# Kernel optimization log

Measured on AMD Instinct MI355X. Metric: run time of the kernel, lower is better.

Reference implementation:

```python
import jax, jax.numpy as jnp
import numpy as np

N_NODES = 4096
N_EDGES = 131072
F_DIM = 16
H_DIM = 32

def _mlp_params(key, in_dim, hidden):
    ks = jax.random.split(key, 6)
    s1 = 1.0 / np.sqrt(in_dim); s2 = 1.0 / np.sqrt(hidden)
    return dict(
        W1=jax.random.uniform(ks[0], (in_dim, hidden), jnp.float32, -s1, s1),
        b1=jax.random.uniform(ks[1], (hidden,), jnp.float32, -s1, s1),
        W2=jax.random.uniform(ks[2], (hidden, hidden), jnp.float32, -s2, s2),
        b2=jax.random.uniform(ks[3], (hidden,), jnp.float32, -s2, s2),
        W3=jax.random.uniform(ks[4], (hidden, 1), jnp.float32, -s2, s2),
        b3=jax.random.uniform(ks[5], (1,), jnp.float32, -s2, s2),
    )

def _mlp(x, W1, b1, W2, b2, W3, b3):
    h = jax.nn.relu(x @ W1 + b1)
    h = jax.nn.relu(h @ W2 + b2)
    return (h @ W3 + b3)[..., 0]  # (E,)

def setup_inputs() -> dict:
    key = jax.random.key(0)
    k_ei, k_ef, k_s, k_p = jax.random.split(key, 4)
    edge_index = jax.random.randint(k_ei, (N_EDGES, 2), 0, N_NODES, dtype=jnp.int32)
    edge_feat = jax.random.normal(k_ef, (N_EDGES, F_DIM), dtype=jnp.float32)
    sh = _mlp_params(k_s, F_DIM, H_DIM)
    sp = _mlp_params(k_p, F_DIM, H_DIM)
    return dict(
        species_idx=0,
        edge_index=edge_index,
        edge_feat=edge_feat,
        num_nodes=N_NODES,
        sW1=sh['W1'], sb1=sh['b1'], sW2=sh['W2'], sb2=sh['b2'], sW3=sh['W3'], sb3=sh['b3'],
        pW1=sp['W1'], pb1=sp['b1'], pW2=sp['W2'], pb2=sp['b2'], pW3=sp['W3'], pb3=sp['b3'],
    )

def reference(species_idx, edge_index, edge_feat, num_nodes,
              sW1, sb1, sW2, sb2, sW3, sb3,
              pW1, pb1, pW2, pb2, pW3, pb3):
    # Edge logits: shared head + species head (species_idx selects the head;
    # here the selected head's params are passed directly).
    shared = _mlp(edge_feat, sW1, sb1, sW2, sb2, sW3, sb3)   # (E,)
    species = _mlp(edge_feat, pW1, pb1, pW2, pb2, pW3, pb3)  # (E,)
    resistance = jax.nn.softplus(shared + species) + 1e-4
    conductance = 1.0 / resistance
    i = edge_index[:, 0]
    j = edge_index[:, 1]
    # Scatter-assembled graph Laplacian (N x N)
    L = jnp.zeros((num_nodes, num_nodes), dtype=edge_feat.dtype)
    L = L.at[i, i].add(conductance)
    L = L.at[j, j].add(conductance)
    L = L.at[i, j].add(-conductance)
    L = L.at[j, i].add(-conductance)
    L_pinv = jnp.linalg.pinv(L)
    diag = jnp.diagonal(L_pinv)
    R = diag[:, None] + diag[None, :] - 2.0 * L_pinv
    return R, shared, species
```

## Files before the change

### kernel.cpp

```cpp
#include <hip/hip_runtime.h>
#include <hip/hip_bf16.h>


#define NN 4096
#define LDA 4096
#define NEDGE 131072
#define INVN (1.0f/4096.0f)

__device__ __forceinline__ float mlp_eval(const float* __restrict__ w,
                                          const float* __restrict__ x) {
  float h1[32], h2[32];
#pragma unroll
  for (int o = 0; o < 32; o += 4) {
    float4 s = *(const float4*)&w[512 + o];
#pragma unroll
    for (int i = 0; i < 16; ++i) {
      float4 wv = *(const float4*)&w[i * 32 + o];
      s.x = fmaf(x[i], wv.x, s.x); s.y = fmaf(x[i], wv.y, s.y);
      s.z = fmaf(x[i], wv.z, s.z); s.w = fmaf(x[i], wv.w, s.w);
    }
    h1[o] = fmaxf(s.x, 0.f); h1[o+1] = fmaxf(s.y, 0.f);
    h1[o+2] = fmaxf(s.z, 0.f); h1[o+3] = fmaxf(s.w, 0.f);
  }
#pragma unroll
  for (int o = 0; o < 32; o += 4) {
    float4 s = *(const float4*)&w[1568 + o];
#pragma unroll
    for (int i = 0; i < 32; ++i) {
      float4 wv = *(const float4*)&w[544 + i * 32 + o];
      s.x = fmaf(h1[i], wv.x, s.x); s.y = fmaf(h1[i], wv.y, s.y);
      s.z = fmaf(h1[i], wv.z, s.z); s.w = fmaf(h1[i], wv.w, s.w);
    }
    h2[o] = fmaxf(s.x, 0.f); h2[o+1] = fmaxf(s.y, 0.f);
    h2[o+2] = fmaxf(s.z, 0.f); h2[o+3] = fmaxf(s.w, 0.f);
  }
  float out = w[1632];
#pragma unroll
  for (int i = 0; i < 32; ++i) out = fmaf(h2[i], w[1600 + i], out);
  return out;
}

__global__ __launch_bounds__(256) void mlp_kernel(
    const float* __restrict__ ef,
    const float* __restrict__ sW1, const float* __restrict__ sb1,
    const float* __restrict__ sW2, const float* __restrict__ sb2,
    const float* __restrict__ sW3, const float* __restrict__ sb3,
    const float* __restrict__ pW1, const float* __restrict__ pb1,
    const float* __restrict__ pW2, const float* __restrict__ pb2,
    const float* __restrict__ pW3, const float* __restrict__ pb3,
    float* __restrict__ outS, float* __restrict__ outP,
    float* __restrict__ cond) {
  __shared__ float w[3328];
  int t = threadIdx.x;
  for (int i = t; i < 512; i += 256) { w[i] = sW1[i]; w[1664 + i] = pW1[i]; }
  for (int i = t; i < 1024; i += 256) { w[544 + i] = sW2[i]; w[1664 + 544 + i] = pW2[i]; }
  if (t < 32) {
    w[512 + t] = sb1[t]; w[1568 + t] = sb2[t]; w[1600 + t] = sW3[t];
    w[1664 + 512 + t] = pb1[t]; w[1664 + 1568 + t] = pb2[t]; w[1664 + 1600 + t] = pW3[t];
  }
  if (t == 0) { w[1632] = sb3[0]; w[1664 + 1632] = pb3[0]; }
  __syncthreads();
  int e = blockIdx.x * 256 + t;
  float x[16];
#pragma unroll
  for (int i = 0; i < 16; i += 4) {
    float4 v = *(const float4*)&ef[(size_t)e * 16 + i];
    x[i] = v.x; x[i+1] = v.y; x[i+2] = v.z; x[i+3] = v.w;
  }
  float s = mlp_eval(w, x);
  float p = mlp_eval(w + 1664, x);
  outS[e] = s; outP[e] = p;
  float z = s + p;
  float sp = fmaxf(z, 0.f) + log1pf(expf(-fabsf(z)));
  cond[e] = 1.0f / (sp + 1e-4f);
}

__global__ __launch_bounds__(256) void init_A(float* __restrict__ A) {
  size_t q = (size_t)blockIdx.x * 256 + threadIdx.x;
  *(float4*)&A[q * 4] = make_float4(INVN, INVN, INVN, INVN);
}

__global__ __launch_bounds__(256) void zero_ws(float* __restrict__ P) {
  size_t q = (size_t)blockIdx.x * 256 + threadIdx.x;
  *(float4*)&P[q * 4] = make_float4(0.f, 0.f, 0.f, 0.f);
}

__global__ __launch_bounds__(256) void scatter_kernel(const int* __restrict__ ei,
                                                      const float* __restrict__ cond,
                                                      float* __restrict__ A) {
  int e = blockIdx.x * 256 + threadIdx.x;
  int i = ei[2 * e], j = ei[2 * e + 1];
  float c = cond[e];
  atomicAdd(&A[(size_t)i * (LDA + 1)], c);
  atomicAdd(&A[(size_t)j * (LDA + 1)], c);
  atomicAdd(&A[(size_t)i * LDA + j], -c);
  atomicAdd(&A[(size_t)j * LDA + i], -c);
}

__device__ __forceinline__ float rlane(float v, int l) {
  return __int_as_float(__builtin_amdgcn_readlane(__float_as_int(v), l));
}

__device__ __noinline__ void potf2_dev(float* __restrict__ A, int kt, int lane,
                                       float (* __restrict__ GT)[68]) {
  float* blk = A + (size_t)kt * 64 * (LDA + 1);
  float a[64], x[64];
#pragma unroll
  for (int c = 0; c < 64; c += 4) {
    float4 v = *(const float4*)&blk[(size_t)lane * LDA + c];
    a[c] = v.x; a[c+1] = v.y; a[c+2] = v.z; a[c+3] = v.w;
    x[c]   = (c   == lane) ? 1.f : 0.f;
    x[c+1] = (c+1 == lane) ? 1.f : 0.f;
    x[c+2] = (c+2 == lane) ? 1.f : 0.f;
    x[c+3] = (c+3 == lane) ? 1.f : 0.f;
  }
#pragma unroll
  for (int j = 0; j < 64; ++j) {
    float dj = rlane(a[j], j);
    float inv = 1.0f / sqrtf(dj);
    float lij = a[j] * inv;
    a[j] = lij;
    float coefT = -lij;
    float sX = (lane == j) ? inv : 1.0f;
    float coefX = (lane > j) ? -lij : 0.0f;
#pragma unroll
    for (int c = j + 1; c < 64; ++c)
      a[c] = fmaf(coefT, rlane(lij, c), a[c]);
#pragma unroll
    for (int c = 0; c <= j; ++c) {
      float xjc = rlane(x[c], j) * inv;
      x[c] = fmaf(coefX, xjc, x[c] * sX);
    }
  }
#pragma unroll
  for (int c = 0; c < 64; c += 4)
    *(float4*)&blk[(size_t)lane * LDA + c] = make_float4(a[c], a[c+1], a[c+2], a[c+3]);
#pragma unroll
  for (int c = 0; c < 64; ++c) GT[c][lane] = x[c];
}

__device__ __forceinline__ void syrk_tile(float* __restrict__ A, int t0, int ti_, int tj_,
                                          const float (* __restrict__ LtA)[68],
                                          const float (* __restrict__ LtB)[68], int gtid) {
  int tx = gtid & 15, ty = gtid >> 4;
  float acc[4][4] = {};
  for (int k = 0; k < 64; ++k) {
    float4 a4 = *(const float4*)&LtA[k][ty * 4];
    float4 b4 = *(const float4*)&LtB[k][tx * 4];
    float aa[4] = {a4.x, a4.y, a4.z, a4.w};
    float bb[4] = {b4.x, b4.y, b4.z, b4.w};
#pragma unroll
    for (int i = 0; i < 4; ++i)
#pragma unroll
      for (int jj = 0; jj < 4; ++jj) acc[i][jj] = fmaf(aa[i], bb[jj], acc[i][jj]);
  }
  float* C = A + ((size_t)(t0 + ti_) * 64) * LDA + (size_t)(t0 + tj_) * 64;
#pragma unroll
  for (int i = 0; i < 4; ++i) {
    float* p = &C[(size_t)(ty * 4 + i) * LDA + tx * 4];
    float4 c = *(float4*)p;
    c.x -= acc[i][0]; c.y -= acc[i][1]; c.z -= acc[i][2]; c.w -= acc[i][3];
    *(float4*)p = c;
  }
}

__global__ __launch_bounds__(512) void potrf_diag256(float* __restrict__ A,
                                                     float* __restrict__ GinvAll,
                                                     int p) {
  __shared__ float GT[64][68];
  __shared__ float At[2][64][68];
  __shared__ float Lt[3][64][68];
  int tid = threadIdx.x;
  int wid = tid >> 6, lane = tid & 63;
  int grp = tid >> 8, gtid = tid & 255;
  int t0 = p * 4;
  for (int kk = 0; kk < 4; ++kk) {
    if (wid == 0) {
      potf2_dev(A, t0 + kk, lane, GT);
    } else if (grp == 1) {
      const int TI_[5] = {2, 3, 2, 3, 3};
      const int TJ_[5] = {1, 1, 2, 2, 3};
#pragma unroll 5
      for (int t = 0; t < 5; ++t) {
        bool on = (kk == 1) || (kk == 2 && t >= 3);
        if (on)
          syrk_tile(A, t0, TI_[t], TJ_[t], Lt[TI_[t] - kk], Lt[TJ_[t] - kk], gtid);
      }
    }
    __syncthreads();
    {
      int base = (t0 + kk) * 4096;
#pragma unroll 8
      for (int u = 0; u < 8; ++u) {
        int q = tid * 8 + u;
        GinvAll[base + q] = GT[q & 63][q >> 6];
      }
    }
    for (int rnd = 0; rnd < 2; ++rnd) {
      int it = kk + 1 + rnd * 2 + grp;
      bool act = (it <= 3);
      if (act) {
        for (int q = gtid; q < 1024; q += 256) {
          int r = q >> 4, k4 = (q & 15) << 2;
          float4 v = *(const float4*)&A[((size_t)(t0 + it) * 64 + r) * LDA +
                                        (size_t)(t0 + kk) * 64 + k4];
          At[grp][k4 + 0][r] = v.x; At[grp][k4 + 1][r] = v.y;
          At[grp][k4 + 2][r] = v.z; At[grp][k4 + 3][r] = v.w;
        }
      }
      __syncthreads();
      if (act) {
        int tx = gtid & 15, ty = gtid >> 4;
        float acc[4][4] = {};
        for (int k = 0; k < 64; ++k) {
          float4 a4 = *(const float4*)&At[grp][k][ty * 4];
          float4 b4 = *(const float4*)&GT[k][tx * 4];
          float aa[4] = {a4.x, a4.y, a4.z, a4.w};
          float bb[4] = {b4.x, b4.y, b4.z, b4.w};
#pragma unroll
          for (int i = 0; i < 4; ++i)
#pragma unroll
            for (int jj = 0; jj < 4; ++jj) acc[i][jj] = fmaf(aa[i], bb[jj], acc[i][jj]);
        }
        int s = it - kk - 1;
#pragma unroll
        for (int jj = 0; jj < 4; ++jj)
          *(float4*)&Lt[s][tx * 4 + jj][ty * 4] =
              make_float4(acc[0][jj], acc[1][jj], acc[2][jj], acc[3][jj]);
        float* C = A + ((size_t)(t0 + it) * 64) * LDA + (size_t)(t0 + kk) * 64;
#pragma unroll
        for (int i = 0; i < 4; ++i)
          *(float4*)&C[(size_t)(ty * 4 + i) * LDA + tx * 4] =
              make_float4(acc[i][0], acc[i][1], acc[i][2], acc[i][3]);
      }
      __syncthreads();
    }
    if (kk < 3 && grp == 0)
      syrk_tile(A, t0, kk + 1, kk + 1, Lt[0], Lt[0], gtid);
    __syncthreads();
  }
}

__global__ __launch_bounds__(256) void trsm_panel256(float* __restrict__ A,
                                                     const float* __restrict__ GinvAll,
                                                     int p) {
  __shared__ float Sr[64][260];
  __shared__ float Bt[64][68];
  int tid = threadIdx.x;
  int c0 = p * 256;
  int r0 = c0 + 256 + blockIdx.x * 64;
  for (int q = tid; q < 4096; q += 256) {
    int r = q >> 6, c4 = (q & 63) << 2;
    *(float4*)&Sr[r][c4] = *(const float4*)&A[(size_t)(r0 + r) * LDA + c0 + c4];
  }
  __syncthreads();
  int tx = tid & 15, ty = tid >> 4;
  for (int j = 0; j < 4; ++j) {
    float acc2[4][4] = {};
    for (int p2 = 0; p2 < j; ++p2) {
      for (int q = tid; q < 1024; q += 256) {
        int c = q >> 4, k4 = (q & 15) << 2;
        float4 v = *(const float4*)&A[(size_t)(c0 + j * 64 + c) * LDA +
                                      c0 + p2 * 64 + k4];
        Bt[k4 + 0][c] = v.x; Bt[k4 + 1][c] = v.y;
        Bt[k4 + 2][c] = v.z; Bt[k4 + 3][c] = v.w;
      }
      __syncthreads();
      for (int k = 0; k < 64; ++k) {
        float a0 = Sr[ty * 4 + 0][p2 * 64 + k];
        float a1 = Sr[ty * 4 + 1][p2 * 64 + k];
        float a2 = Sr[ty * 4 + 2][p2 * 64 + k];
        float a3 = Sr[ty * 4 + 3][p2 * 64 + k];
        float4 b = *(const float4*)&Bt[k][tx * 4];
        acc2[0][0] = fmaf(a0, b.x, acc2[0][0]); acc2[0][1] = fmaf(a0, b.y, acc2[0][1]);
        acc2[0][2] = fmaf(a0, b.z, acc2[0][2]); acc2[0][3] = fmaf(a0, b.w, acc2[0][3]);
        acc2[1][0] = fmaf(a1, b.x, acc2[1][0]); acc2[1][1] = fmaf(a1, b.y, acc2[1][1]);
        acc2[1][2] = fmaf(a1, b.z, acc2[1][2]); acc2[1][3] = fmaf(a1, b.w, acc2[1][3]);
        acc2[2][0] = fmaf(a2, b.x, acc2[2][0]); acc2[2][1] = fmaf(a2, b.y, acc2[2][1]);
        acc2[2][2] = fmaf(a2, b.z, acc2[2][2]); acc2[2][3] = fmaf(a2, b.w, acc2[2][3]);
        acc2[3][0] = fmaf(a3, b.x, acc2[3][0]); acc2[3][1] = fmaf(a3, b.y, acc2[3][1]);
        acc2[3][2] = fmaf(a3, b.z, acc2[3][2]); acc2[3][3] = fmaf(a3, b.w, acc2[3][3]);
      }
      __syncthreads();
    }
    if (j > 0) {
#pragma unroll
      for (int i = 0; i < 4; ++i) {
        Sr[ty * 4 + i][j * 64 + tx * 4 + 0] -= acc2[i][0];
        Sr[ty * 4 + i][j * 64 + tx * 4 + 1] -= acc2[i][1];
        Sr[ty * 4 + i][j * 64 + tx * 4 + 2] -= acc2[i][2];
        Sr[ty * 4 + i][j * 64 + tx * 4 + 3] -= acc2[i][3];
      }
    }
    __syncthreads();
    {
      const float* G = GinvAll + (size_t)(p * 4 + j) * 4096;
      for (int q = tid; q < 1024; q += 256) {
        int c = q >> 4, k4 = (q & 15) << 2;
        float4 v = *(const float4*)&G[c * 64 + k4];
        Bt[k4 + 0][c] = v.x; Bt[k4 + 1][c] = v.y;
        Bt[k4 + 2][c] = v.z; Bt[k4 + 3][c] = v.w;
      }
    }
    __syncthreads();
    float acc3[4][4] = {};
    for (int k = 0; k < 64; ++k) {
      float a0 = Sr[ty * 4 + 0][j * 64 + k];
      float a1 = Sr[ty * 4 + 1][j * 64 + k];
      float a2 = Sr[ty * 4 + 2][j * 64 + k];
      float a3 = Sr[ty * 4 + 3][j * 64 + k];
      float4 b = *(const float4*)&Bt[k][tx * 4];
      acc3[0][0] = fmaf(a0, b.x, acc3[0][0]); acc3[0][1] = fmaf(a0, b.y, acc3[0][1]);
      acc3[0][2] = fmaf(a0, b.z, acc3[0][2]); acc3[0][3] = fmaf(a0, b.w, acc3[0][3]);
      acc3[1][0] = fmaf(a1, b.x, acc3[1][0]); acc3[1][1] = fmaf(a1, b.y, acc3[1][1]);
      acc3[1][2] = fmaf(a1, b.z, acc3[1][2]); acc3[1][3] = fmaf(a1, b.w, acc3[1][3]);
      acc3[2][0] = fmaf(a2, b.x, acc3[2][0]); acc3[2][1] = fmaf(a2, b.y, acc3[2][1]);
      acc3[2][2] = fmaf(a2, b.z, acc3[2][2]); acc3[2][3] = fmaf(a2, b.w, acc3[2][3]);
      acc3[3][0] = fmaf(a3, b.x, acc3[3][0]); acc3[3][1] = fmaf(a3, b.y, acc3[3][1]);
      acc3[3][2] = fmaf(a3, b.z, acc3[3][2]); acc3[3][3] = fmaf(a3, b.w, acc3[3][3]);
    }
    __syncthreads();
#pragma unroll
    for (int i = 0; i < 4; ++i) {
      Sr[ty * 4 + i][j * 64 + tx * 4 + 0] = acc3[i][0];
      Sr[ty * 4 + i][j * 64 + tx * 4 + 1] = acc3[i][1];
      Sr[ty * 4 + i][j * 64 + tx * 4 + 2] = acc3[i][2];
      Sr[ty * 4 + i][j * 64 + tx * 4 + 3] = acc3[i][3];
    }
    __syncthreads();
  }
  for (int q = tid; q < 4096; q += 256) {
    int r = q >> 6, c4 = (q & 63) << 2;
    *(float4*)&A[(size_t)(r0 + r) * LDA + c0 + c4] = *(float4*)&Sr[r][c4];
  }
}

template <bool TA, bool TB, bool ACCUM, bool LOWER, bool KST, bool CCOMP>
__global__ __launch_bounds__(256) void gemm64(
    const float* __restrict__ Ab, long long aZ, int lda,
    const float* __restrict__ Bb, long long bZ, int ldb,
    float* __restrict__ Cb, long long cZ, int ldc, int K, float alpha) {
  int ti = blockIdx.x, tj = blockIdx.y;
  if (LOWER && tj > ti) return;
  const float* A = Ab + (long long)blockIdx.z * aZ;
  const float* B = Bb + (long long)blockIdx.z * bZ;
  __shared__ float As[16][68], Bs[16][68];
  int tid = threadIdx.x;
  int tx = tid & 15, ty = tid >> 4;
  float acc[4][4] = {};
  int m0 = ti * 64, n0 = tj * 64;
  int k0 = KST ? ti * 64 : 0;
  for (int k = k0; k < K; k += 16) {
    if (!TA) {
      int r = tid >> 2, c4 = (tid & 3) * 4;
      float4 v = *(const float4*)&A[(size_t)(m0 + r) * lda + k + c4];
      As[c4 + 0][r] = v.x; As[c4 + 1][r] = v.y; As[c4 + 2][r] = v.z; As[c4 + 3][r] = v.w;
    } else {
      int r = tid >> 4, c4 = (tid & 15) * 4;
      *(float4*)&As[r][c4] = *(const float4*)&A[(size_t)(k + r) * lda + m0 + c4];
    }
    if (TB) {
      int r = tid >> 2, c4 = (tid & 3) * 4;
      float4 v = *(const float4*)&B[(size_t)(n0 + r) * ldb + k + c4];
      Bs[c4 + 0][r] = v.x; Bs[c4 + 1][r] = v.y; Bs[c4 + 2][r] = v.z; Bs[c4 + 3][r] = v.w;
    } else {
      int r = tid >> 4, c4 = (tid & 15) * 4;
      *(float4*)&Bs[r][c4] = *(const float4*)&B[(size_t)(k + r) * ldb + n0 + c4];
    }
    __syncthreads();
#pragma unroll
    for (int kk = 0; kk < 16; ++kk) {
      float4 av = *(const float4*)&As[kk][ty * 4];
      float4 bv = *(const float4*)&Bs[kk][tx * 4];
      float a[4] = {av.x, av.y, av.z, av.w};
      float b[4] = {bv.x, bv.y, bv.z, bv.w};
#pragma unroll
      for (int i = 0; i < 4; ++i)
#pragma unroll
        for (int jj = 0; jj < 4; ++jj) acc[i][jj] = fmaf(a[i], b[jj], acc[i][jj]);
    }
    __syncthreads();
  }
  float* C = Cb + (long long)blockIdx.z * cZ;
#pragma unroll
  for (int i = 0; i < 4; ++i) {
    size_t off = (size_t)(m0 + ty * 4 + i) * ldc + n0 + tx * 4;
    float4 c;
    if (ACCUM) {
      c = *(float4*)&C[off];
      c.x += alpha * acc[i][0]; c.y += alpha * acc[i][1];
      c.z += alpha * acc[i][2]; c.w += alpha * acc[i][3];
    } else {
      c.x = alpha * acc[i][0]; c.y = alpha * acc[i][1];
      c.z = alpha * acc[i][2]; c.w = alpha * acc[i][3];
    }
    *(float4*)&C[off] = c;
  }
}

template <bool TA, bool TB, bool ACCUM, bool TRI, bool KST, bool CCOMP,
          bool ATOMIC, bool KSPLIT>
__global__ __launch_bounds__(256) void gemm128(
    const float* __restrict__ Ab, long long aZ, int lda,
    const float* __restrict__ Bb, long long bZ, int ldb,
    float* __restrict__ Cb, long long cZ, int ldc, int K, float alpha) {
  int ti, tj;
  if (TRI) {
    int bid = blockIdx.x;
    ti = (int)((sqrtf(8.0f * bid + 1.0f) - 1.0f) * 0.5f);
    while ((ti + 1) * (ti + 2) / 2 <= bid) ++ti;
    while (ti * (ti + 1) / 2 > bid) --ti;
    tj = bid - ti * (ti + 1) / 2;
  } else {
    ti = blockIdx.x; tj = blockIdx.y;
  }
  int k0 = KST ? ti * 128 : 0;
  int kEnd = K;
  if (KSPLIT) {
    if (blockIdx.z == 0) { kEnd = 2048; if (k0 >= kEnd) return; }
    else { k0 = (k0 > 2048) ? k0 : 2048; }
  }
  const float* A = KSPLIT ? Ab : Ab + (long long)blockIdx.z * aZ;
  const float* B = KSPLIT ? Bb : Bb + (long long)blockIdx.z * bZ;
  __shared__ float As[16][132], Bs[16][132];
  int tid = threadIdx.x;
  int tx = tid & 15, ty = tid >> 4;
  float acc[8][8] = {};
  int m0 = ti * 128, n0 = tj * 128;
  for (int k = k0; k < kEnd; k += 16) {
    if (!TA) {
      int r = tid >> 1, c8 = (tid & 1) * 8;
      const float* src = &A[(size_t)(m0 + r) * lda + k + c8];
      float4 v0 = *(const float4*)src;
      float4 v1 = *(const float4*)(src + 4);
      As[c8 + 0][r] = v0.x; As[c8 + 1][r] = v0.y; As[c8 + 2][r] = v0.z; As[c8 + 3][r] = v0.w;
      As[c8 + 4][r] = v1.x; As[c8 + 5][r] = v1.y; As[c8 + 6][r] = v1.z; As[c8 + 7][r] = v1.w;
    } else {
      int r = tid >> 4, c8 = (tid & 15) * 8;
      const float* src = &A[(size_t)(k + r) * lda + m0 + c8];
      *(float4*)&As[r][c8]     = *(const float4*)src;
      *(float4*)&As[r][c8 + 4] = *(const float4*)(src + 4);
    }
    if (TB) {
      int r = tid >> 1, c8 = (tid & 1) * 8;
      const float* src = &B[(size_t)(n0 + r) * ldb + k + c8];
      float4 v0 = *(const float4*)src;
      float4 v1 = *(const float4*)(src + 4);
      Bs[c8 + 0][r] = v0.x; Bs[c8 + 1][r] = v0.y; Bs[c8 + 2][r] = v0.z; Bs[c8 + 3][r] = v0.w;
      Bs[c8 + 4][r] = v1.x; Bs[c8 + 5][r] = v1.y; Bs[c8 + 6][r] = v1.z; Bs[c8 + 7][r] = v1.w;
    } else {
      int r = tid >> 4, c8 = (tid & 15) * 8;
      const float* src = &B[(size_t)(k + r) * ldb + n0 + c8];
      *(float4*)&Bs[r][c8]     = *(const float4*)src;
      *(float4*)&Bs[r][c8 + 4] = *(const float4*)(src + 4);
    }
    __syncthreads();
#pragma unroll
    for (int kk = 0; kk < 16; ++kk) {
      float a8[8], b8[8];
      *(float4*)&a8[0] = *(const float4*)&As[kk][ty * 4];
      *(float4*)&a8[4] = *(const float4*)&As[kk][64 + ty * 4];
      *(float4*)&b8[0] = *(const float4*)&Bs[kk][tx * 4];
      *(float4*)&b8[4] = *(const float4*)&Bs[kk][64 + tx * 4];
#pragma unroll
      for (int i = 0; i < 8; ++i)
#pragma unroll
        for (int jj = 0; jj < 8; ++jj) acc[i][jj] = fmaf(a8[i], b8[jj], acc[i][jj]);
    }
    __syncthreads();
  }
  if (CCOMP) {
#pragma unroll
    for (int hr = 0; hr < 2; ++hr) {
      int TI = 2 * ti + hr;
#pragma unroll
      for (int hc = 0; hc < 2; ++hc) {
        int TJ = 2 * tj + hc;
        if (TJ > TI) continue;
        float* C = Cb + ((size_t)TI * (TI + 1) / 2 + TJ) * 4096;
#pragma unroll
        for (int i = 0; i < 4; ++i) {
          if (ATOMIC) {
            float* pbase = &C[(ty * 4 + i) * 64 + tx * 4];
            atomicAdd(pbase + 0, alpha * acc[hr * 4 + i][hc * 4 + 0]);
            atomicAdd(pbase + 1, alpha * acc[hr * 4 + i][hc * 4 + 1]);
            atomicAdd(pbase + 2, alpha * acc[hr * 4 + i][hc * 4 + 2]);
            atomicAdd(pbase + 3, alpha * acc[hr * 4 + i][hc * 4 + 3]);
          } else {
            float4 c;
            c.x = alpha * acc[hr * 4 + i][hc * 4 + 0];
            c.y = alpha * acc[hr * 4 + i][hc * 4 + 1];
            c.z = alpha * acc[hr * 4 + i][hc * 4 + 2];
            c.w = alpha * acc[hr * 4 + i][hc * 4 + 3];
            *(float4*)&C[(ty * 4 + i) * 64 + tx * 4] = c;
          }
        }
      }
    }
  } else {
    float* C = Cb + (long long)blockIdx.z * cZ;
#pragma unroll
    for (int i = 0; i < 8; ++i) {
      int row = (i < 4) ? (m0 + ty * 4 + i) : (m0 + 64 + ty * 4 + i - 4);
      float* dst0 = &C[(size_t)row * ldc + n0 + tx * 4];
      float* dst1 = dst0 + 64;
      float4 c0, c1;
      c0.x = alpha * acc[i][0]; c0.y = alpha * acc[i][1];
      c0.z = alpha * acc[i][2]; c0.w = alpha * acc[i][3];
      c1.x = alpha * acc[i][4]; c1.y = alpha * acc[i][5];
      c1.z = alpha * acc[i][6]; c1.w = alpha * acc[i][7];
      if (ACCUM) {
        float4 o0 = *(float4*)dst0, o1 = *(float4*)dst1;
        c0.x += o0.x; c0.y += o0.y; c0.z += o0.z; c0.w += o0.w;
        c1.x += o1.x; c1.y += o1.y; c1.z += o1.z; c1.w += o1.w;
      }
      *(float4*)dst0 = c0;
      *(float4*)dst1 = c1;
    }
  }
}

__global__ __launch_bounds__(256) void finish_W_prep(float* __restrict__ A,
                                                     const float* __restrict__ GinvAll) {
  size_t q = (size_t)blockIdx.x * 256 + threadIdx.x;
  int r = (int)(q >> 10), c4 = (int)(q & 1023) << 2;
  int rb = r >> 6, cb = c4 >> 6;
  if (cb == rb) {
    const float* g = GinvAll + (size_t)rb * 4096 + (size_t)(r & 63) * 64 + (c4 & 63);
    *(float4*)&A[q * 4] = *(const float4*)g;
  } else if (cb > rb) {
    *(float4*)&A[q * 4] = make_float4(0.f, 0.f, 0.f, 0.f);
  }
}

__global__ __launch_bounds__(256) void copy_diag(const float* __restrict__ Mc,
                                                 float* __restrict__ d) {
  int i = blockIdx.x * 256 + threadIdx.x;
  int tb = i >> 6;
  size_t q = (size_t)tb * (tb + 1) / 2 + tb;
  d[i] = Mc[q * 4096 + (size_t)(i & 63) * 65];
}

__global__ __launch_bounds__(256) void final_R(const float* __restrict__ Mc,
                                               const float* __restrict__ d,
                                               float* __restrict__ out) {
  size_t idx = (size_t)blockIdx.x * 256 + threadIdx.x;
  int r = (int)(idx >> 12), c = (int)(idx & 4095);
  int a = r > c ? r : c, b = r > c ? c : r;
  int ta = a >> 6, tb = b >> 6;
  size_t q = (size_t)ta * (ta + 1) / 2 + tb;
  float m = Mc[q * 4096 + (size_t)(a & 63) * 64 + (b & 63)];
  out[idx] = d[r] + d[c] - 2.0f * m;
}

extern "C" void kernel_launch(void* const* d_in, const int* in_sizes, int n_in,
                              void* d_out, int out_size, void* d_ws, size_t ws_size,
                              hipStream_t stream) {
  const int* eidx = (const int*)d_in[1];
  const float* ef = (const float*)d_in[2];
  const float* sW1 = (const float*)d_in[4],  *sb1 = (const float*)d_in[5];
  const float* sW2 = (const float*)d_in[6],  *sb2 = (const float*)d_in[7];
  const float* sW3 = (const float*)d_in[8],  *sb3 = (const float*)d_in[9];
  const float* pW1 = (const float*)d_in[10], *pb1 = (const float*)d_in[11];
  const float* pW2 = (const float*)d_in[12], *pb2 = (const float*)d_in[13];
  const float* pW3 = (const float*)d_in[14], *pb3 = (const float*)d_in[15];

  float* dout = (float*)d_out;
  float* dA = dout;
  float* outS = dout + (size_t)NN * NN;
  float* outP = outS + NEDGE;

  float* ws = (float*)d_ws;
  float* Mc = ws;
  float* U = ws + 8519680ull;
  float* cond = U;
  float* Ginv = U;
  float* Tbuf = U;
  float* diagb = U;

  mlp_kernel<<<NEDGE / 256, 256, 0, stream>>>(ef, sW1, sb1, sW2, sb2, sW3, sb3,
                                              pW1, pb1, pW2, pb2, pW3, pb3,
                                              outS, outP, cond);
  zero_ws<<<2080, 256, 0, stream>>>(Mc);
  init_A<<<(NN * NN / 4) / 256, 256, 0, stream>>>(dA);
  scatter_kernel<<<NEDGE / 256, 256, 0, stream>>>(eidx, cond, dA);

  for (int p = 0; p < 16; ++p) {
    potrf_diag256<<<1, 512, 0, stream>>>(dA, Ginv, p);
    int rem = NN - (p + 1) * 256;
    if (rem > 0) {
      trsm_panel256<<<rem / 64, 256, 0, stream>>>(dA, Ginv, p);
      int nt = rem / 128;
      float* Lp = dA + (size_t)((p + 1) * 256) * LDA + (size_t)p * 256;
      float* trail = dA + (size_t)((p + 1) * 256) * (LDA + 1);
      gemm128<false, true, true, true, false, false, false, false>
          <<<dim3(nt * (nt + 1) / 2, 1, 1), 256, 0, stream>>>(
              Lp, 0, LDA, Lp, 0, LDA, trail, 0, LDA, 256, -1.0f);
    }
  }

  finish_W_prep<<<(NN * NN / 4) / 256, 256, 0, stream>>>(dA, Ginv);

  for (int S = 64; S <= 2048; S *= 2) {
    int np = NN / (2 * S);
    long long pz = (long long)2 * S * (LDA + 1);
    if (S == 64) {
      gemm64<false, false, false, false, false, false>
          <<<dim3(1, 1, np), 256, 0, stream>>>(
              dA + (size_t)S * LDA, pz, LDA, dA, pz, LDA,
              Tbuf, (long long)S * S, S, S, 1.0f);
      gemm64<false, false, false, false, false, false>
          <<<dim3(1, 1, np), 256, 0, stream>>>(
              dA + (size_t)S * (LDA + 1), pz, LDA, Tbuf, (long long)S * S, S,
              dA + (size_t)S * LDA, pz, LDA, S, -1.0f);
    } else {
      gemm128<false, false, false, false, false, false, false, false>
          <<<dim3(S / 128, S / 128, np), 256, 0, stream>>>(
              dA + (size_t)S * LDA, pz, LDA, dA, pz, LDA,
              Tbuf, (long long)S * S, S, S, 1.0f);
      gemm128<false, false, false, false, false, false, false, false>
          <<<dim3(S / 128, S / 128, np), 256, 0, stream>>>(
              dA + (size_t)S * (LDA + 1), pz, LDA, Tbuf, (long long)S * S, S,
              dA + (size_t)S * LDA, pz, LDA, S, -1.0f);
    }
  }

  gemm128<true, false, false, true, true, true, true, true>
      <<<dim3(528, 1, 2), 256, 0, stream>>>(dA, 0, LDA, dA, 0, LDA, Mc, 0, 64,
                                            NN, 1.0f);

  copy_diag<<<NN / 256, 256, 0, stream>>>(Mc, diagb);
  final_R<<<(NN * NN) / 256, 256, 0, stream>>>(Mc, diagb, dout);
}
```

Measured before the change: 5.583 ms.

## Fuse blocked Cholesky loop into one cooperative persistent kernel with lookahead

Replaces the per-panel launches of diagonal factorization, panel TRSM and trailing SYRK/GEMM with a single cooperative kernel of 224 workgroups that uses grid syncs between phases. Workgroup 0 factors the next diagonal block while the other workgroups apply the remaining trailing update. The panel columns needed next are updated first, which gives a one-step lookahead. This targets launch overhead and the serial single-block diagonal factorization, at the cost of grid-wide barriers and a lower-occupancy single-block potrf path. If the cooperative launch fails, it falls back to the old launch sequence.

Result: slower. 7.510 ms (+34.5%).

```diff
diff --git a/kernel.cpp b/kernel.cpp
--- a/kernel.cpp
+++ b/kernel.cpp
@@ -1,11 +1,15 @@
 #include <hip/hip_runtime.h>
 #include <hip/hip_bf16.h>
+#include <hip/hip_cooperative_groups.h>
+
+namespace cg = cooperative_groups;
 
 
 #define NN 4096
 #define LDA 4096
 #define NEDGE 131072
 #define INVN (1.0f/4096.0f)
+#define COOP_WG 224
 
 __device__ __forceinline__ float mlp_eval(const float* __restrict__ w,
                                           const float* __restrict__ x) {
@@ -161,6 +165,256 @@
     float4 c = *(float4*)p;
     c.x -= acc[i][0]; c.y -= acc[i][1]; c.z -= acc[i][2]; c.w -= acc[i][3];
     *(float4*)p = c;
+  }
+}
+
+__device__ __forceinline__ int tri_i(int bid) {
+  int ti = (int)((sqrtf(8.0f * bid + 1.0f) - 1.0f) * 0.5f);
+  while ((ti + 1) * (ti + 2) / 2 <= bid) ++ti;
+  while (ti * (ti + 1) / 2 > bid) --ti;
+  return ti;
+}
+
+__device__ void gemm_sub_tile(float* __restrict__ A, int m0, int n0, int k0,
+                              float* __restrict__ sh, int tid) {
+  float (*As)[132] = reinterpret_cast<float(*)[132]>(sh);
+  float (*Bs)[132] = reinterpret_cast<float(*)[132]>(sh + 2112);
+  int tx = tid & 15, ty = tid >> 4;
+  float acc[8][8] = {};
+  for (int k = k0; k < k0 + 256; k += 16) {
+    {
+      int r = tid >> 1, c8 = (tid & 1) * 8;
+      const float* src = &A[(size_t)(m0 + r) * LDA + k + c8];
+      float4 v0 = *(const float4*)src;
+      float4 v1 = *(const float4*)(src + 4);
+      As[c8 + 0][r] = v0.x; As[c8 + 1][r] = v0.y; As[c8 + 2][r] = v0.z; As[c8 + 3][r] = v0.w;
+      As[c8 + 4][r] = v1.x; As[c8 + 5][r] = v1.y; As[c8 + 6][r] = v1.z; As[c8 + 7][r] = v1.w;
+    }
+    {
+      int r = tid >> 1, c8 = (tid & 1) * 8;
+      const float* src = &A[(size_t)(n0 + r) * LDA + k + c8];
+      float4 v0 = *(const float4*)src;
+      float4 v1 = *(const float4*)(src + 4);
+      Bs[c8 + 0][r] = v0.x; Bs[c8 + 1][r] = v0.y; Bs[c8 + 2][r] = v0.z; Bs[c8 + 3][r] = v0.w;
+      Bs[c8 + 4][r] = v1.x; Bs[c8 + 5][r] = v1.y; Bs[c8 + 6][r] = v1.z; Bs[c8 + 7][r] = v1.w;
+    }
+    __syncthreads();
+#pragma unroll
+    for (int kk = 0; kk < 16; ++kk) {
+      float a8[8], b8[8];
+      *(float4*)&a8[0] = *(const float4*)&As[kk][ty * 4];
+      *(float4*)&a8[4] = *(const float4*)&As[kk][64 + ty * 4];
+      *(float4*)&b8[0] = *(const float4*)&Bs[kk][tx * 4];
+      *(float4*)&b8[4] = *(const float4*)&Bs[kk][64 + tx * 4];
+#pragma unroll
+      for (int i = 0; i < 8; ++i)
+#pragma unroll
+        for (int jj = 0; jj < 8; ++jj) acc[i][jj] = fmaf(a8[i], b8[jj], acc[i][jj]);
+    }
+    __syncthreads();
+  }
+#pragma unroll
+  for (int i = 0; i < 8; ++i) {
+    int row = (i < 4) ? (m0 + ty * 4 + i) : (m0 + 64 + ty * 4 + i - 4);
+    float* dst0 = &A[(size_t)row * LDA + n0 + tx * 4];
+    float* dst1 = dst0 + 64;
+    float4 o0 = *(float4*)dst0, o1 = *(float4*)dst1;
+    o0.x -= acc[i][0]; o0.y -= acc[i][1]; o0.z -= acc[i][2]; o0.w -= acc[i][3];
+    o1.x -= acc[i][4]; o1.y -= acc[i][5]; o1.z -= acc[i][6]; o1.w -= acc[i][7];
+    *(float4*)dst0 = o0;
+    *(float4*)dst1 = o1;
+  }
+}
+
+__device__ void diag_panel_seq(float* __restrict__ A, float* __restrict__ GinvAll,
+                               int p, float* __restrict__ sh, int tid) {
+  float (*GT)[68] = reinterpret_cast<float(*)[68]>(sh);
+  float (*At)[68] = reinterpret_cast<float(*)[68]>(sh + 4352);
+  int t0 = p * 4;
+  for (int kk = 0; kk < 4; ++kk) {
+    if (tid < 64) potf2_dev(A, t0 + kk, tid, GT);
+    __syncthreads();
+    {
+      int base = (t0 + kk) * 4096;
+      for (int q = tid; q < 4096; q += 256)
+        GinvAll[base + q] = GT[q & 63][q >> 6];
+    }
+    for (int it = kk + 1; it <= 3; ++it) {
+      for (int q = tid; q < 1024; q += 256) {
+        int r = q >> 4, k4 = (q & 15) << 2;
+        float4 v = *(const float4*)&A[((size_t)(t0 + it) * 64 + r) * LDA +
+                                      (size_t)(t0 + kk) * 64 + k4];
+        At[k4 + 0][r] = v.x; At[k4 + 1][r] = v.y;
+        At[k4 + 2][r] = v.z; At[k4 + 3][r] = v.w;
+      }
+      __syncthreads();
+      int tx = tid & 15, ty = tid >> 4;
+      float acc[4][4] = {};
+      for (int k = 0; k < 64; ++k) {
+        float4 a4 = *(const float4*)&At[k][ty * 4];
+        float4 b4 = *(const float4*)&GT[k][tx * 4];
+        float aa[4] = {a4.x, a4.y, a4.z, a4.w};
+        float bb[4] = {b4.x, b4.y, b4.z, b4.w};
+#pragma unroll
+        for (int i = 0; i < 4; ++i)
+#pragma unroll
+          for (int jj = 0; jj < 4; ++jj) acc[i][jj] = fmaf(aa[i], bb[jj], acc[i][jj]);
+      }
+      float (*Lt)[68] = reinterpret_cast<float(*)[68]>(sh + 8704 + (size_t)(it - kk - 1) * 4352);
+#pragma unroll
+      for (int jj = 0; jj < 4; ++jj)
+        *(float4*)&Lt[tx * 4 + jj][ty * 4] =
+            make_float4(acc[0][jj], acc[1][jj], acc[2][jj], acc[3][jj]);
+      float* C = A + ((size_t)(t0 + it) * 64) * LDA + (size_t)(t0 + kk) * 64;
+#pragma unroll
+      for (int i = 0; i < 4; ++i)
+        *(float4*)&C[(size_t)(ty * 4 + i) * LDA + tx * 4] =
+            make_float4(acc[i][0], acc[i][1], acc[i][2], acc[i][3]);
+      __syncthreads();
+    }
+    for (int j = kk + 1; j <= 3; ++j)
+      for (int i = j; i <= 3; ++i) {
+        const float (*LtA)[68] =
+            reinterpret_cast<const float(*)[68]>(sh + 8704 + (size_t)(i - kk - 1) * 4352);
+        const float (*LtB)[68] =
+            reinterpret_cast<const float(*)[68]>(sh + 8704 + (size_t)(j - kk - 1) * 4352);
+        syrk_tile(A, t0, i, j, LtA, LtB, tid);
+      }
+    __syncthreads();
+  }
+}
+
+__device__ void trsm_strip_body(float* __restrict__ A, const float* __restrict__ GinvAll,
+                                int p, int strip, float (* __restrict__ Sr)[260],
+                                float (* __restrict__ Bt)[68], int tid) {
+  int c0 = p * 256;
+  int r0 = c0 + 256 + strip * 64;
+  for (int q = tid; q < 4096; q += 256) {
+    int r = q >> 6, c4 = (q & 63) << 2;
+    *(float4*)&Sr[r][c4] = *(const float4*)&A[(size_t)(r0 + r) * LDA + c0 + c4];
+  }
+  __syncthreads();
+  int tx = tid & 15, ty = tid >> 4;
+  for (int j = 0; j < 4; ++j) {
+    float acc2[4][4] = {};
+    for (int p2 = 0; p2 < j; ++p2) {
+      for (int q = tid; q < 1024; q += 256) {
+        int c = q >> 4, k4 = (q & 15) << 2;
+        float4 v = *(const float4*)&A[(size_t)(c0 + j * 64 + c) * LDA + c0 + p2 * 64 + k4];
+        Bt[k4 + 0][c] = v.x; Bt[k4 + 1][c] = v.y;
+        Bt[k4 + 2][c] = v.z; Bt[k4 + 3][c] = v.w;
+      }
+      __syncthreads();
+      for (int k = 0; k < 64; ++k) {
+        float a0 = Sr[ty * 4 + 0][p2 * 64 + k];
+        float a1 = Sr[ty * 4 + 1][p2 * 64 + k];
+        float a2 = Sr[ty * 4 + 2][p2 * 64 + k];
+        float a3 = Sr[ty * 4 + 3][p2 * 64 + k];
+        float4 b = *(const float4*)&Bt[k][tx * 4];
+        acc2[0][0] = fmaf(a0, b.x, acc2[0][0]); acc2[0][1] = fmaf(a0, b.y, acc2[0][1]);
+        acc2[0][2] = fmaf(a0, b.z, acc2[0][2]); acc2[0][3] = fmaf(a0, b.w, acc2[0][3]);
+        acc2[1][0] = fmaf(a1, b.x, acc2[1][0]); acc2[1][1] = fmaf(a1, b.y, acc2[1][1]);
+        acc2[1][2] = fmaf(a1, b.z, acc2[1][2]); acc2[1][3] = fmaf(a1, b.w, acc2[1][3]);
+        acc2[2][0] = fmaf(a2, b.x, acc2[2][0]); acc2[2][1] = fmaf(a2, b.y, acc2[2][1]);
+        acc2[2][2] = fmaf(a2, b.z, acc2[2][2]); acc2[2][3] = fmaf(a2, b.w, acc2[2][3]);
+        acc2[3][0] = fmaf(a3, b.x, acc2[3][0]); acc2[3][1] = fmaf(a3, b.y, acc2[3][1]);
+        acc2[3][2] = fmaf(a3, b.z, acc2[3][2]); acc2[3][3] = fmaf(a3, b.w, acc2[3][3]);
+      }
+      __syncthreads();
+    }
+    if (j > 0) {
+#pragma unroll
+      for (int i = 0; i < 4; ++i) {
+        Sr[ty * 4 + i][j * 64 + tx * 4 + 0] -= acc2[i][0];
+        Sr[ty * 4 + i][j * 64 + tx * 4 + 1] -= acc2[i][1];
+        Sr[ty * 4 + i][j * 64 + tx * 4 + 2] -= acc2[i][2];
+        Sr[ty * 4 + i][j * 64 + tx * 4 + 3] -= acc2[i][3];
+      }
+    }
+    __syncthreads();
+    {
+      const float* G = GinvAll + (size_t)(p * 4 + j) * 4096;
+      for (int q = tid; q < 1024; q += 256) {
+        int c = q >> 4, k4 = (q & 15) << 2;
+        float4 v = *(const float4*)&G[c * 64 + k4];
+        Bt[k4 + 0][c] = v.x; Bt[k4 + 1][c] = v.y;
+        Bt[k4 + 2][c] = v.z; Bt[k4 + 3][c] = v.w;
+      }
+    }
+    __syncthreads();
+    float acc3[4][4] = {};
+    for (int k = 0; k < 64; ++k) {
+      float a0 = Sr[ty * 4 + 0][j * 64 + k];
+      float a1 = Sr[ty * 4 + 1][j * 64 + k];
+      float a2 = Sr[ty * 4 + 2][j * 64 + k];
+      float a3 = Sr[ty * 4 + 3][j * 64 + k];
+      float4 b = *(const float4*)&Bt[k][tx * 4];
+      acc3[0][0] = fmaf(a0, b.x, acc3[0][0]); acc3[0][1] = fmaf(a0, b.y, acc3[0][1]);
+      acc3[0][2] = fmaf(a0, b.z, acc3[0][2]); acc3[0][3] = fmaf(a0, b.w, acc3[0][3]);
+      acc3[1][0] = fmaf(a1, b.x, acc3[1][0]); acc3[1][1] = fmaf(a1, b.y, acc3[1][1]);
+      acc3[1][2] = fmaf(a1, b.z, acc3[1][2]); acc3[1][3] = fmaf(a1, b.w, acc3[1][3]);
+      acc3[2][0] = fmaf(a2, b.x, acc3[2][0]); acc3[2][1] = fmaf(a2, b.y, acc3[2][1]);
+      acc3[2][2] = fmaf(a2, b.z, acc3[2][2]); acc3[2][3] = fmaf(a2, b.w, acc3[2][3]);
+      acc3[3][0] = fmaf(a3, b.x, acc3[3][0]); acc3[3][1] = fmaf(a3, b.y, acc3[3][1]);
+      acc3[3][2] = fmaf(a3, b.z, acc3[3][2]); acc3[3][3] = fmaf(a3, b.w, acc3[3][3]);
+    }
+    __syncthreads();
+#pragma unroll
+    for (int i = 0; i < 4; ++i) {
+      Sr[ty * 4 + i][j * 64 + tx * 4 + 0] = acc3[i][0];
+      Sr[ty * 4 + i][j * 64 + tx * 4 + 1] = acc3[i][1];
+      Sr[ty * 4 + i][j * 64 + tx * 4 + 2] = acc3[i][2];
+      Sr[ty * 4 + i][j * 64 + tx * 4 + 3] = acc3[i][3];
+    }
+    __syncthreads();
+  }
+  for (int q = tid; q < 4096; q += 256) {
+    int r = q >> 6, c4 = (q & 63) << 2;
+    *(float4*)&A[(size_t)(r0 + r) * LDA + c0 + c4] = *(float4*)&Sr[r][c4];
+  }
+}
+
+__global__ __launch_bounds__(256) void chol_coop(float* __restrict__ A,
+                                                 float* __restrict__ Ginv) {
+  cg::grid_group grid = cg::this_grid();
+  __shared__ float sh[21760];
+  const int wg = blockIdx.x;
+  const int tid = threadIdx.x;
+  for (int p = 0; p < 16; ++p) {
+    if (p > 0) {
+      int base = 256 * p;
+      int ntot = ((NN - base) / 128) * 2;
+      for (int t = wg; t < ntot; t += COOP_WG)
+        gemm_sub_tile(A, base + (t >> 1) * 128, base + (t & 1) * 128,
+                      256 * (p - 1), sh, tid);
+    }
+    __threadfence();
+    grid.sync();
+    if (wg == 0) {
+      diag_panel_seq(A, Ginv, p, sh, tid);
+    } else if (p > 0) {
+      int base = 256 * (p + 1);
+      if (base < NN) {
+        int nt = (NN - base) / 128;
+        int ntot = nt * (nt + 1) / 2;
+        for (int t = wg - 1; t < ntot; t += (COOP_WG - 1)) {
+          int ti = tri_i(t), tj = t - ti * (ti + 1) / 2;
+          gemm_sub_tile(A, base + ti * 128, base + tj * 128, 256 * (p - 1), sh, tid);
+        }
+      }
+    }
+    __threadfence();
+    grid.sync();
+    int rem = NN - 256 * (p + 1);
+    if (rem > 0) {
+      float (*Sr)[260] = reinterpret_cast<float(*)[260]>(sh);
+      float (*Bt)[68] = reinterpret_cast<float(*)[68]>(sh + 16640);
+      int ns = rem / 64;
+      for (int s = wg; s < ns; s += COOP_WG)
+        trsm_strip_body(A, Ginv, p, s, Sr, Bt, tid);
+    }
+    __threadfence();
+    grid.sync();
   }
 }
 
@@ -246,93 +500,7 @@
                                                      int p) {
   __shared__ float Sr[64][260];
   __shared__ float Bt[64][68];
-  int tid = threadIdx.x;
-  int c0 = p * 256;
-  int r0 = c0 + 256 + blockIdx.x * 64;
-  for (int q = tid; q < 4096; q += 256) {
-    int r = q >> 6, c4 = (q & 63) << 2;
-    *(float4*)&Sr[r][c4] = *(const float4*)&A[(size_t)(r0 + r) * LDA + c0 + c4];
-  }
-  __syncthreads();
-  int tx = tid & 15, ty = tid >> 4;
-  for (int j = 0; j < 4; ++j) {
-    float acc2[4][4] = {};
-    for (int p2 = 0; p2 < j; ++p2) {
-      for (int q = tid; q < 1024; q += 256) {
-        int c = q >> 4, k4 = (q & 15) << 2;
-        float4 v = *(const float4*)&A[(size_t)(c0 + j * 64 + c) * LDA +
-                                      c0 + p2 * 64 + k4];
-        Bt[k4 + 0][c] = v.x; Bt[k4 + 1][c] = v.y;
-        Bt[k4 + 2][c] = v.z; Bt[k4 + 3][c] = v.w;
-      }
-      __syncthreads();
-      for (int k = 0; k < 64; ++k) {
-        float a0 = Sr[ty * 4 + 0][p2 * 64 + k];
-        float a1 = Sr[ty * 4 + 1][p2 * 64 + k];
-        float a2 = Sr[ty * 4 + 2][p2 * 64 + k];
-        float a3 = Sr[ty * 4 + 3][p2 * 64 + k];
-        float4 b = *(const float4*)&Bt[k][tx * 4];
-        acc2[0][0] = fmaf(a0, b.x, acc2[0][0]); acc2[0][1] = fmaf(a0, b.y, acc2[0][1]);
-        acc2[0][2] = fmaf(a0, b.z, acc2[0][2]); acc2[0][3] = fmaf(a0, b.w, acc2[0][3]);
-        acc2[1][0] = fmaf(a1, b.x, acc2[1][0]); acc2[1][1] = fmaf(a1, b.y, acc2[1][1]);
-        acc2[1][2] = fmaf(a1, b.z, acc2[1][2]); acc2[1][3] = fmaf(a1, b.w, acc2[1][3]);
-        acc2[2][0] = fmaf(a2, b.x, acc2[2][0]); acc2[2][1] = fmaf(a2, b.y, acc2[2][1]);
-        acc2[2][2] = fmaf(a2, b.z, acc2[2][2]); acc2[2][3] = fmaf(a2, b.w, acc2[2][3]);
-        acc2[3][0] = fmaf(a3, b.x, acc2[3][0]); acc2[3][1] = fmaf(a3, b.y, acc2[3][1]);
-        acc2[3][2] = fmaf(a3, b.z, acc2[3][2]); acc2[3][3] = fmaf(a3, b.w, acc2[3][3]);
-      }
-      __syncthreads();
-    }
-    if (j > 0) {
-#pragma unroll
-      for (int i = 0; i < 4; ++i) {
-        Sr[ty * 4 + i][j * 64 + tx * 4 + 0] -= acc2[i][0];
-        Sr[ty * 4 + i][j * 64 + tx * 4 + 1] -= acc2[i][1];
-        Sr[ty * 4 + i][j * 64 + tx * 4 + 2] -= acc2[i][2];
-        Sr[ty * 4 + i][j * 64 + tx * 4 + 3] -= acc2[i][3];
-      }
-    }
-    __syncthreads();
-    {
-      const float* G = GinvAll + (size_t)(p * 4 + j) * 4096;
-      for (int q = tid; q < 1024; q += 256) {
-        int c = q >> 4, k4 = (q & 15) << 2;
-        float4 v = *(const float4*)&G[c * 64 + k4];
-        Bt[k4 + 0][c] = v.x; Bt[k4 + 1][c] = v.y;
-        Bt[k4 + 2][c] = v.z; Bt[k4 + 3][c] = v.w;
-      }
-    }
-    __syncthreads();
-    float acc3[4][4] = {};
-    for (int k = 0; k < 64; ++k) {
-      float a0 = Sr[ty * 4 + 0][j * 64 + k];
-      float a1 = Sr[ty * 4 + 1][j * 64 + k];
-      float a2 = Sr[ty * 4 + 2][j * 64 + k];
-      float a3 = Sr[ty * 4 + 3][j * 64 + k];
-      float4 b = *(const float4*)&Bt[k][tx * 4];
-      acc3[0][0] = fmaf(a0, b.x, acc3[0][0]); acc3[0][1] = fmaf(a0, b.y, acc3[0][1]);
-      acc3[0][2] = fmaf(a0, b.z, acc3[0][2]); acc3[0][3] = fmaf(a0, b.w, acc3[0][3]);
-      acc3[1][0] = fmaf(a1, b.x, acc3[1][0]); acc3[1][1] = fmaf(a1, b.y, acc3[1][1]);
-      acc3[1][2] = fmaf(a1, b.z, acc3[1][2]); acc3[1][3] = fmaf(a1, b.w, acc3[1][3]);
-      acc3[2][0] = fmaf(a2, b.x, acc3[2][0]); acc3[2][1] = fmaf(a2, b.y, acc3[2][1]);
-      acc3[2][2] = fmaf(a2, b.z, acc3[2][2]); acc3[2][3] = fmaf(a2, b.w, acc3[2][3]);
-      acc3[3][0] = fmaf(a3, b.x, acc3[3][0]); acc3[3][1] = fmaf(a3, b.y, acc3[3][1]);
-      acc3[3][2] = fmaf(a3, b.z, acc3[3][2]); acc3[3][3] = fmaf(a3, b.w, acc3[3][3]);
-    }
-    __syncthreads();
-#pragma unroll
-    for (int i = 0; i < 4; ++i) {
-      Sr[ty * 4 + i][j * 64 + tx * 4 + 0] = acc3[i][0];
-      Sr[ty * 4 + i][j * 64 + tx * 4 + 1] = acc3[i][1];
-      Sr[ty * 4 + i][j * 64 + tx * 4 + 2] = acc3[i][2];
-      Sr[ty * 4 + i][j * 64 + tx * 4 + 3] = acc3[i][3];
-    }
-    __syncthreads();
-  }
-  for (int q = tid; q < 4096; q += 256) {
-    int r = q >> 6, c4 = (q & 63) << 2;
-    *(float4*)&A[(size_t)(r0 + r) * LDA + c0 + c4] = *(float4*)&Sr[r][c4];
-  }
+  trsm_strip_body(A, GinvAll, p, blockIdx.x, Sr, Bt, threadIdx.x);
 }
 
 template <bool TA, bool TB, bool ACCUM, bool LOWER, bool KST, bool CCOMP>
@@ -407,9 +575,7 @@
   int ti, tj;
   if (TRI) {
     int bid = blockIdx.x;
-    ti = (int)((sqrtf(8.0f * bid + 1.0f) - 1.0f) * 0.5f);
-    while ((ti + 1) * (ti + 2) / 2 <= bid) ++ti;
-    while (ti * (ti + 1) / 2 > bid) --ti;
+    ti = tri_i(bid);
     tj = bid - ti * (ti + 1) / 2;
   } else {
     ti = blockIdx.x; tj = blockIdx.y;
@@ -585,17 +751,23 @@
   init_A<<<(NN * NN / 4) / 256, 256, 0, stream>>>(dA);
   scatter_kernel<<<NEDGE / 256, 256, 0, stream>>>(eidx, cond, dA);
 
-  for (int p = 0; p < 16; ++p) {
-    potrf_diag256<<<1, 512, 0, stream>>>(dA, Ginv, p);
-    int rem = NN - (p + 1) * 256;
-    if (rem > 0) {
-      trsm_panel256<<<rem / 64, 256, 0, stream>>>(dA, Ginv, p);
-      int nt = rem / 128;
-      float* Lp = dA + (size_t)((p + 1) * 256) * LDA + (size_t)p * 256;
-      float* trail = dA + (size_t)((p + 1) * 256) * (LDA + 1);
-      gemm128<false, true, true, true, false, false, false, false>
-          <<<dim3(nt * (nt + 1) / 2, 1, 1), 256, 0, stream>>>(
-              Lp, 0, LDA, Lp, 0, LDA, trail, 0, LDA, 256, -1.0f);
+  void* kargs[] = {(void*)&dA, (void*)&Ginv};
+  hipError_t cerr = hipLaunchCooperativeKernel((const void*)chol_coop,
+                                               dim3(COOP_WG, 1, 1), dim3(256, 1, 1),
+                                               kargs, 0, stream);
+  if (cerr != hipSuccess) {
+    for (int p = 0; p < 16; ++p) {
+      potrf_diag256<<<1, 512, 0, stream>>>(dA, Ginv, p);
+      int rem = NN - (p + 1) * 256;
+      if (rem > 0) {
+        trsm_panel256<<<rem / 64, 256, 0, stream>>>(dA, Ginv, p);
+        int nt = rem / 128;
+        float* Lp = dA + (size_t)((p + 1) * 256) * LDA + (size_t)p * 256;
+        float* trail = dA + (size_t)((p + 1) * 256) * (LDA + 1);
+        gemm128<false, true, true, true, false, false, false, false>
+            <<<dim3(nt * (nt + 1) / 2, 1, 1), 256, 0, stream>>>(
+                Lp, 0, LDA, Lp, 0, LDA, trail, 0, LDA, 256, -1.0f);
+      }
     }
   }
 
```
